# Optimization experiments

Measured on AMD Instinct MI355X. Metric: run time of the kernel, lower is better.

Reference implementation:

```python
import jax, jax.numpy as jnp
import numpy as np

N = 100000   # nodes
E = 1600000  # edges
DIN, DH, DOUT = 64, 128, 128


def setup_inputs() -> dict:
    key = jax.random.key(0)
    ks = jax.random.split(key, 12)
    x = jax.random.normal(ks[0], (N, DIN), dtype=jnp.float32)
    edge_index = jax.random.randint(ks[1], (2, E), 0, N, dtype=jnp.int32)
    s = 1.0 / np.sqrt(DIN)
    W1 = jax.random.uniform(ks[2], (DIN, DH), jnp.float32, -s, s)
    b1 = jnp.zeros((DH,), jnp.float32)
    g1 = jnp.ones((DH,), jnp.float32)
    bt1 = jnp.zeros((DH,), jnp.float32)
    s2 = 1.0 / np.sqrt(DH)
    W2 = jax.random.uniform(ks[3], (DH, DOUT), jnp.float32, -s2, s2)
    b2 = jnp.zeros((DOUT,), jnp.float32)
    g2 = jnp.ones((DOUT,), jnp.float32)
    bt2 = jnp.zeros((DOUT,), jnp.float32)
    return {"x": x, "edge_index": edge_index, "W1": W1, "b1": b1, "g1": g1,
            "bt1": bt1, "W2": W2, "b2": b2, "g2": g2, "bt2": bt2}


def _layer_norm(h, g, b, eps=1e-5):
    mu = h.mean(-1, keepdims=True)
    var = h.var(-1, keepdims=True)
    return (h - mu) * jax.lax.rsqrt(var + eps) * g + b


def reference(x, edge_index, W1, b1, g1, bt1, W2, b2, g2, bt2):
    # GCN normalization with self-loops (shared graph structure for both layers)
    src, dst = edge_index[0], edge_index[1]
    loops = jnp.arange(N, dtype=src.dtype)
    src = jnp.concatenate([src, loops])
    dst = jnp.concatenate([dst, loops])
    deg = jax.ops.segment_sum(jnp.ones_like(src, jnp.float32), dst, num_segments=N)
    dinv = jnp.where(deg > 0, jax.lax.rsqrt(deg), 0.0)
    norm = dinv[src] * dinv[dst]  # [E+N]

    def gcn(h, W, b):
        hw = h @ W                         # linear first (PyG GCNConv)
        msg = hw[src] * norm[:, None]      # gather + edge scale
        return jax.ops.segment_sum(msg, dst, num_segments=N) + b

    h = jax.nn.relu(_layer_norm(gcn(x, W1, b1), g1, bt1))
    # dropout is identity at inference
    h = jax.nn.relu(_layer_norm(gcn(h, W2, b2), g2, bt2))
    return h
```

## Files before the change

kernel.cpp:

```cpp
#include <hip/hip_runtime.h>

#define NN 100000
#define NE 1600000
#define NBKT 196
#define CAP 12288
#define EPB 8192
#define ABLK ((NE + EPB - 1) / EPB)
typedef unsigned short u16;
typedef unsigned int u32;

typedef __attribute__((ext_vector_type(8))) short short8v;
typedef __attribute__((ext_vector_type(4))) float f32x4;

__device__ __forceinline__ u32 f2bf(float f) {
    u32 u = __float_as_uint(f);
    return (u + 0x7fffu + ((u >> 16) & 1u)) >> 16;
}
__device__ __forceinline__ u32 pack2(float a, float b) {
    return f2bf(a) | (f2bf(b) << 16);
}
__device__ __forceinline__ void accum8(float* a, uint4 u, float w) {
    a[0] += __uint_as_float(u.x << 16) * w;
    a[1] += __uint_as_float(u.x & 0xffff0000u) * w;
    a[2] += __uint_as_float(u.y << 16) * w;
    a[3] += __uint_as_float(u.y & 0xffff0000u) * w;
    a[4] += __uint_as_float(u.z << 16) * w;
    a[5] += __uint_as_float(u.z & 0xffff0000u) * w;
    a[6] += __uint_as_float(u.w << 16) * w;
    a[7] += __uint_as_float(u.w & 0xffff0000u) * w;
}

__global__ __launch_bounds__(256) void kA_bin(const int* __restrict__ src,
                                              const int* __restrict__ dst,
                                              int* __restrict__ gcnt,
                                              u32* __restrict__ binned) {
    __shared__ int bc[NBKT];
    __shared__ int cbase[NBKT];
    const int tid = threadIdx.x;
    for (int i = tid; i < NBKT; i += 256) bc[i] = 0;
    __syncthreads();
    const int e0 = blockIdx.x * EPB;
#pragma unroll
    for (int i = 0; i < EPB / 256; ++i) {
        const int e = e0 + i * 256 + tid;
        if (e < NE) atomicAdd(&bc[dst[e] >> 9], 1);
    }
    __syncthreads();
    for (int i = tid; i < NBKT; i += 256)
        cbase[i] = bc[i] ? atomicAdd(&gcnt[i], bc[i]) : 0;
    __syncthreads();
    for (int i = tid; i < NBKT; i += 256) bc[i] = 0;
    __syncthreads();
#pragma unroll
    for (int i = 0; i < EPB / 256; ++i) {
        const int e = e0 + i * 256 + tid;
        if (e < NE) {
            const int d = dst[e];
            const int bkt = d >> 9;
            const int p = atomicAdd(&bc[bkt], 1);
            binned[bkt * CAP + cbase[bkt] + p] = ((u32)src[e] << 9) | (u32)(d & 511);
        }
    }
}

__global__ __launch_bounds__(256) void kB_fill(const u32* __restrict__ binned,
                                               const int* __restrict__ gcnt,
                                               int2* __restrict__ off2,
                                               float* __restrict__ dinv,
                                               int* __restrict__ csr) {
    __shared__ int lcnt[512];
    __shared__ int lpos[512];
    __shared__ int ws[4];
    const int b = blockIdx.x;
    const int tid = threadIdx.x;
    const int cnt = gcnt[b];
    const int base0 = b * CAP;
    const int node0 = b << 9;
    lcnt[tid] = 0;
    lcnt[tid + 256] = 0;
    __syncthreads();
    for (int e = tid; e < cnt; e += 256)
        atomicAdd(&lcnt[binned[base0 + e] & 511], 1);
    __syncthreads();
    const int c0 = lcnt[tid * 2], c1 = lcnt[tid * 2 + 1];
    const int s = c0 + c1;
    const int lane = tid & 63, w = tid >> 6;
    int incl = s;
#pragma unroll
    for (int o = 1; o < 64; o <<= 1) {
        const int u = __shfl_up(incl, o);
        if (lane >= o) incl += u;
    }
    if (lane == 63) ws[w] = incl;
    __syncthreads();
    int base = incl - s;
    for (int i = 0; i < w; ++i) base += ws[i];
    lpos[tid * 2] = base;
    lpos[tid * 2 + 1] = base + c0;
    const int n0 = node0 + tid * 2;
    if (n0 < NN) {
        off2[n0] = make_int2(base0 + base, base0 + base + c0);
        dinv[n0] = rsqrtf(1.0f + (float)c0);
    }
    if (n0 + 1 < NN) {
        off2[n0 + 1] = make_int2(base0 + base + c0, base0 + base + c0 + c1);
        dinv[n0 + 1] = rsqrtf(1.0f + (float)c1);
    }
    __syncthreads();
    for (int e = tid; e < cnt; e += 256) {
        const u32 u = binned[base0 + e];
        const int p = atomicAdd(&lpos[u & 511], 1);
        csr[base0 + p] = (int)(u >> 9);
    }
}

__global__ __launch_bounds__(256) void k_cvt(const float* __restrict__ x,
                                             const float* __restrict__ dinv,
                                             u16* __restrict__ xb) {
    const int i = blockIdx.x * 256 + threadIdx.x;
    if (i < NN * 8) {
        const int row = i >> 3;
        const float dr = dinv[row];
        const float4 v0 = *(const float4*)&x[(size_t)i * 8];
        const float4 v1 = *(const float4*)&x[(size_t)i * 8 + 4];
        uint4 o;
        o.x = pack2(v0.x * dr, v0.y * dr); o.y = pack2(v0.z * dr, v0.w * dr);
        o.z = pack2(v1.x * dr, v1.y * dr); o.w = pack2(v1.z * dr, v1.w * dr);
        *(uint4*)&xb[(size_t)i * 8] = o;
    }
}

__global__ __launch_bounds__(256) void k_wt(const float* __restrict__ W,
                                            u16* __restrict__ WT, int K) {
    const int i = blockIdx.x * 256 + threadIdx.x;
    if (i < K * 128) {
        const int k = i >> 7, c = i & 127;
        WT[c * K + k] = (u16)f2bf(W[i]);
    }
}

__global__ __launch_bounds__(256) void k_agg64(const u16* __restrict__ A,
                                               const int2* __restrict__ off2,
                                               const int* __restrict__ csr,
                                               const float* __restrict__ dinv,
                                               u16* __restrict__ out) {
    const int node = blockIdx.x * 4 + (threadIdx.x >> 6);
    const int lane = threadIdx.x & 63;
    const int sub = lane >> 3, l = lane & 7;
    const u32 coff = (u32)l << 4;
    const char* Ab = (const char*)A;
    const float di = dinv[node];
    float a[8] = {};
    {
        const uint4 u = *(const uint4*)(Ab + (u32)node * 128u + coff);
        accum8(a, u, (sub == 0) ? 1.0f : 0.0f);
    }
    const int2 oe = off2[node];
    int base = oe.x;
    const int e1 = oe.y;
    u32 iA = 0, iB = 0;
    float vA = 0.f, vB = 0.f;
    if (base < e1) {
        const int eA = base + sub, eB = base + sub + 8;
        iA = (u32)csr[min(eA, e1 - 1)];
        iB = (u32)csr[min(eB, e1 - 1)];
        vA = (eA < e1) ? 1.f : 0.f;
        vB = (eB < e1) ? 1.f : 0.f;
    }
    while (base < e1) {
        const uint4 uA = *(const uint4*)(Ab + iA * 128u + coff);
        const uint4 uB = *(const uint4*)(Ab + iB * 128u + coff);
        const float wA = vA, wB = vB;
        base += 16;
        if (base < e1) {
            const int eA = base + sub, eB = base + sub + 8;
            iA = (u32)csr[min(eA, e1 - 1)];
            iB = (u32)csr[min(eB, e1 - 1)];
            vA = (eA < e1) ? 1.f : 0.f;
            vB = (eB < e1) ? 1.f : 0.f;
        }
        accum8(a, uA, wA);
        accum8(a, uB, wB);
    }
#pragma unroll
    for (int i = 0; i < 8; ++i) {
        a[i] += __shfl_xor(a[i], 8);
        a[i] += __shfl_xor(a[i], 16);
        a[i] += __shfl_xor(a[i], 32);
    }
    if (sub == 0) {
        uint4 o;
        o.x = pack2(a[0] * di, a[1] * di); o.y = pack2(a[2] * di, a[3] * di);
        o.z = pack2(a[4] * di, a[5] * di); o.w = pack2(a[6] * di, a[7] * di);
        *(uint4*)((char*)out + (u32)node * 128u + coff) = o;
    }
}

__global__ __launch_bounds__(256) void k_agg128(const u16* __restrict__ A,
                                                const int2* __restrict__ off2,
                                                const int* __restrict__ csr,
                                                const float* __restrict__ dinv,
                                                u16* __restrict__ out) {
    const int node = blockIdx.x * 4 + (threadIdx.x >> 6);
    const int lane = threadIdx.x & 63;
    const int sub = lane >> 4, l = lane & 15;
    const u32 coff = (u32)l << 4;
    const char* Ab = (const char*)A;
    const float di = dinv[node];
    float a[8] = {};
    {
        const uint4 u = *(const uint4*)(Ab + ((u32)node << 8) + coff);
        accum8(a, u, (sub == 0) ? 1.0f : 0.0f);
    }
    const int2 oe = off2[node];
    int base = oe.x;
    const int e1 = oe.y;
    u32 iA = 0, iB = 0;
    float vA = 0.f, vB = 0.f;
    if (base < e1) {
        const int eA = base + sub, eB = base + sub + 4;
        iA = (u32)csr[min(eA, e1 - 1)];
        iB = (u32)csr[min(eB, e1 - 1)];
        vA = (eA < e1) ? 1.f : 0.f;
        vB = (eB < e1) ? 1.f : 0.f;
    }
    while (base < e1) {
        const uint4 uA = *(const uint4*)(Ab + (iA << 8) + coff);
        const uint4 uB = *(const uint4*)(Ab + (iB << 8) + coff);
        const float wA = vA, wB = vB;
        base += 8;
        if (base < e1) {
            const int eA = base + sub, eB = base + sub + 4;
            iA = (u32)csr[min(eA, e1 - 1)];
            iB = (u32)csr[min(eB, e1 - 1)];
            vA = (eA < e1) ? 1.f : 0.f;
            vB = (eB < e1) ? 1.f : 0.f;
        }
        accum8(a, uA, wA);
        accum8(a, uB, wB);
    }
#pragma unroll
    for (int i = 0; i < 8; ++i) {
        a[i] += __shfl_xor(a[i], 16);
        a[i] += __shfl_xor(a[i], 32);
    }
    if (sub == 0) {
        uint4 o;
        o.x = pack2(a[0] * di, a[1] * di); o.y = pack2(a[2] * di, a[3] * di);
        o.z = pack2(a[4] * di, a[5] * di); o.w = pack2(a[6] * di, a[7] * di);
        *(uint4*)((char*)out + ((u32)node << 8) + coff) = o;
    }
}

template<int K, bool FP32OUT, bool PRESCALE>
__global__ __launch_bounds__(256) void k_gemm_ln(const u16* __restrict__ Ain,
                                                 const u16* __restrict__ WT,
                                                 const float* __restrict__ bias,
                                                 const float* __restrict__ g,
                                                 const float* __restrict__ bt,
                                                 const float* __restrict__ dinv,
                                                 void* __restrict__ outp) {
    const int tid = threadIdx.x;
    const int wv = tid >> 6, lane = tid & 63;
    const int lr = lane & 15, kg = lane >> 4;
    const int row0 = blockIdx.x * 128 + wv * 32;

    short8v af[2][K / 32];
#pragma unroll
    for (int rt = 0; rt < 2; ++rt) {
        const int r = min(row0 + rt * 16 + lr, NN - 1);
#pragma unroll
        for (int kk = 0; kk < K / 32; ++kk)
            af[rt][kk] = *(const short8v*)&Ain[(size_t)r * K + kk * 32 + kg * 8];
    }
    f32x4 acc[2][8];
#pragma unroll
    for (int rt = 0; rt < 2; ++rt)
#pragma unroll
        for (int nt = 0; nt < 8; ++nt)
            acc[rt][nt] = (f32x4){0.f, 0.f, 0.f, 0.f};

#pragma unroll
    for (int nt = 0; nt < 8; ++nt) {
        const int col = nt * 16 + lr;
        short8v bf[K / 32];
#pragma unroll
        for (int kk = 0; kk < K / 32; ++kk)
            bf[kk] = *(const short8v*)&WT[col * K + kk * 32 + kg * 8];
#pragma unroll
        for (int rt = 0; rt < 2; ++rt)
#pragma unroll
            for (int kk = 0; kk < K / 32; ++kk)
                acc[rt][nt] = __builtin_amdgcn_mfma_f32_16x16x32_bf16(
                    af[rt][kk], bf[kk], acc[rt][nt], 0, 0, 0);
    }

    float bv[8], gv[8], tv[8];
#pragma unroll
    for (int nt = 0; nt < 8; ++nt) {
        const int col = nt * 16 + lr;
        bv[nt] = bias[col]; gv[nt] = g[col]; tv[nt] = bt[col];
    }

#pragma unroll
    for (int rt = 0; rt < 2; ++rt) {
        float s1[4] = {0.f, 0.f, 0.f, 0.f};
        float s2[4] = {0.f, 0.f, 0.f, 0.f};
#pragma unroll
        for (int nt = 0; nt < 8; ++nt)
#pragma unroll
            for (int j = 0; j < 4; ++j) {
                const float v = acc[rt][nt][j] + bv[nt];
                acc[rt][nt][j] = v;
                s1[j] += v;
                s2[j] += v * v;
            }
#pragma unroll
        for (int j = 0; j < 4; ++j)
#pragma unroll
            for (int o = 1; o < 16; o <<= 1) {
                s1[j] += __shfl_xor(s1[j], o);
                s2[j] += __shfl_xor(s2[j], o);
            }
#pragma unroll
        for (int j = 0; j < 4; ++j) {
            const int r = row0 + rt * 16 + kg * 4 + j;
            const float mu = s1[j] * (1.0f / 128.0f);
            const float var = s2[j] * (1.0f / 128.0f) - mu * mu;
            const float rs = rsqrtf(var + 1e-5f);
            if (r < NN) {
                const float dr = PRESCALE ? dinv[r] : 1.0f;
#pragma unroll
                for (int nt = 0; nt < 8; ++nt) {
                    const float y = fmaxf((acc[rt][nt][j] - mu) * rs * gv[nt] + tv[nt], 0.f) * dr;
                    const int col = nt * 16 + lr;
                    if constexpr (FP32OUT)
                        ((float*)outp)[(size_t)r * 128 + col] = y;
                    else
                        ((u16*)outp)[(size_t)r * 128 + col] = (u16)f2bf(y);
                }
            }
        }
    }
}

extern "C" void kernel_launch(void* const* d_in, const int* in_sizes, int n_in,
                              void* d_out, int out_size, void* d_ws, size_t ws_size,
                              hipStream_t stream) {
    const float* x   = (const float*)d_in[0];
    const int*   ei  = (const int*)d_in[1];
    const float* W1  = (const float*)d_in[2];
    const float* b1  = (const float*)d_in[3];
    const float* g1  = (const float*)d_in[4];
    const float* bt1 = (const float*)d_in[5];
    const float* W2  = (const float*)d_in[6];
    const float* b2  = (const float*)d_in[7];
    const float* g2  = (const float*)d_in[8];
    const float* bt2 = (const float*)d_in[9];

    const int* src = ei;
    const int* dst = ei + NE;

    const int NP = (NN + 255) & ~255;
    int*   gcnt  = (int*)d_ws;
    int2*  off2  = (int2*)(gcnt + 256);
    float* dinv  = (float*)(off2 + NP);
    int*   csr   = (int*)(dinv + NP);
    u32*   binR  = (u32*)(csr + NBKT * CAP);
    u16*   xb    = (u16*)(binR + (size_t)NN * 32);
    u16*   aggh  = xb + (size_t)NN * 64;
    u16*   WT1   = aggh + (size_t)NN * 128;
    u16*   WT2   = WT1 + 128 * 64;
    u32*   binned = binR;
    u16*   aggx  = (u16*)binR;
    u16*   h1    = (u16*)d_out;

    hipMemsetAsync(gcnt, 0, NBKT * sizeof(int), stream);
    kA_bin<<<ABLK, 256, 0, stream>>>(src, dst, gcnt, binned);
    kB_fill<<<NBKT, 256, 0, stream>>>(binned, gcnt, off2, dinv, csr);

    k_cvt<<<(NN * 8 + 255) / 256, 256, 0, stream>>>(x, dinv, xb);
    k_wt<<<(64 * 128 + 255) / 256, 256, 0, stream>>>(W1, WT1, 64);
    k_wt<<<(128 * 128 + 255) / 256, 256, 0, stream>>>(W2, WT2, 128);

    k_agg64<<<NN / 4, 256, 0, stream>>>(xb, off2, csr, dinv, aggx);
    k_gemm_ln<64, false, true><<<(NN + 127) / 128, 256, 0, stream>>>(
        aggx, WT1, b1, g1, bt1, dinv, h1);

    k_agg128<<<NN / 4, 256, 0, stream>>>(h1, off2, csr, dinv, aggh);
    k_gemm_ln<128, true, false><<<(NN + 127) / 128, 256, 0, stream>>>(
        aggh, WT2, b2, g2, bt2, dinv, d_out);
}
```

Baseline: 216.4 us.

## Pad CSR rows to multiples of four and gather four neighbors per lane

```diff
diff --git a/kernel.cpp b/kernel.cpp
--- a/kernel.cpp
+++ b/kernel.cpp
@@ -28,6 +28,16 @@
     a[5] += __uint_as_float(u.z & 0xffff0000u) * w;
     a[6] += __uint_as_float(u.w << 16) * w;
     a[7] += __uint_as_float(u.w & 0xffff0000u) * w;
+}
+__device__ __forceinline__ void accum8a(float* a, uint4 u) {
+    a[0] += __uint_as_float(u.x << 16);
+    a[1] += __uint_as_float(u.x & 0xffff0000u);
+    a[2] += __uint_as_float(u.y << 16);
+    a[3] += __uint_as_float(u.y & 0xffff0000u);
+    a[4] += __uint_as_float(u.z << 16);
+    a[5] += __uint_as_float(u.z & 0xffff0000u);
+    a[6] += __uint_as_float(u.w << 16);
+    a[7] += __uint_as_float(u.w & 0xffff0000u);
 }
 
 __global__ __launch_bounds__(256) void kA_bin(const int* __restrict__ src,
@@ -83,7 +93,9 @@
         atomicAdd(&lcnt[binned[base0 + e] & 511], 1);
     __syncthreads();
     const int c0 = lcnt[tid * 2], c1 = lcnt[tid * 2 + 1];
-    const int s = c0 + c1;
+    const int a0 = (c0 + 3) & ~3;
+    const int a1 = (c1 + 3) & ~3;
+    const int s = a0 + a1;
     const int lane = tid & 63, w = tid >> 6;
     int incl = s;
 #pragma unroll
@@ -96,16 +108,20 @@
     int base = incl - s;
     for (int i = 0; i < w; ++i) base += ws[i];
     lpos[tid * 2] = base;
-    lpos[tid * 2 + 1] = base + c0;
+    lpos[tid * 2 + 1] = base + a0;
     const int n0 = node0 + tid * 2;
     if (n0 < NN) {
         off2[n0] = make_int2(base0 + base, base0 + base + c0);
         dinv[n0] = rsqrtf(1.0f + (float)c0);
     }
     if (n0 + 1 < NN) {
-        off2[n0 + 1] = make_int2(base0 + base + c0, base0 + base + c0 + c1);
+        off2[n0 + 1] = make_int2(base0 + base + a0, base0 + base + a0 + c1);
         dinv[n0 + 1] = rsqrtf(1.0f + (float)c1);
     }
+    for (int k = c0; k < a0; ++k) csr[base0 + base + k] = 0;
+    for (int k = c1; k < a1; ++k) csr[base0 + base + a0 + k] = 0;
+    const int total = ws[0] + ws[1] + ws[2] + ws[3];
+    if (tid < 32) csr[base0 + total + tid] = 0;
     __syncthreads();
     for (int e = tid; e < cnt; e += 256) {
         const u32 u = binned[base0 + e];
@@ -147,40 +163,32 @@
     const int node = blockIdx.x * 4 + (threadIdx.x >> 6);
     const int lane = threadIdx.x & 63;
     const int sub = lane >> 3, l = lane & 7;
-    const u32 coff = (u32)l << 4;
-    const char* Ab = (const char*)A;
+    const char* Ab = (const char*)A + ((u32)l << 4);
     const float di = dinv[node];
     float a[8] = {};
     {
-        const uint4 u = *(const uint4*)(Ab + (u32)node * 128u + coff);
+        const uint4 u = *(const uint4*)(Ab + ((u32)node << 7));
         accum8(a, u, (sub == 0) ? 1.0f : 0.0f);
     }
     const int2 oe = off2[node];
-    int base = oe.x;
+    int e = oe.x;
     const int e1 = oe.y;
-    u32 iA = 0, iB = 0;
-    float vA = 0.f, vB = 0.f;
-    if (base < e1) {
-        const int eA = base + sub, eB = base + sub + 8;
-        iA = (u32)csr[min(eA, e1 - 1)];
-        iB = (u32)csr[min(eB, e1 - 1)];
-        vA = (eA < e1) ? 1.f : 0.f;
-        vB = (eB < e1) ? 1.f : 0.f;
-    }
-    while (base < e1) {
-        const uint4 uA = *(const uint4*)(Ab + iA * 128u + coff);
-        const uint4 uB = *(const uint4*)(Ab + iB * 128u + coff);
-        const float wA = vA, wB = vB;
-        base += 16;
-        if (base < e1) {
-            const int eA = base + sub, eB = base + sub + 8;
-            iA = (u32)csr[min(eA, e1 - 1)];
-            iB = (u32)csr[min(eB, e1 - 1)];
-            vA = (eA < e1) ? 1.f : 0.f;
-            vB = (eB < e1) ? 1.f : 0.f;
+    while (e < e1) {
+        const int4 ce = *(const int4*)&csr[e + 4 * sub];
+        const uint4 u0 = *(const uint4*)(Ab + ((u32)ce.x << 7));
+        const uint4 u1 = *(const uint4*)(Ab + ((u32)ce.y << 7));
+        const uint4 u2 = *(const uint4*)(Ab + ((u32)ce.z << 7));
+        const uint4 u3 = *(const uint4*)(Ab + ((u32)ce.w << 7));
+        if (e + 32 <= e1) {
+            accum8a(a, u0); accum8a(a, u1); accum8a(a, u2); accum8a(a, u3);
+        } else {
+            const int eb = e + 4 * sub;
+            accum8(a, u0, (eb + 0 < e1) ? 1.f : 0.f);
+            accum8(a, u1, (eb + 1 < e1) ? 1.f : 0.f);
+            accum8(a, u2, (eb + 2 < e1) ? 1.f : 0.f);
+            accum8(a, u3, (eb + 3 < e1) ? 1.f : 0.f);
         }
-        accum8(a, uA, wA);
-        accum8(a, uB, wB);
+        e += 32;
     }
 #pragma unroll
     for (int i = 0; i < 8; ++i) {
@@ -192,7 +200,7 @@
         uint4 o;
         o.x = pack2(a[0] * di, a[1] * di); o.y = pack2(a[2] * di, a[3] * di);
         o.z = pack2(a[4] * di, a[5] * di); o.w = pack2(a[6] * di, a[7] * di);
-        *(uint4*)((char*)out + (u32)node * 128u + coff) = o;
+        *(uint4*)((char*)out + ((u32)node << 7) + ((u32)l << 4)) = o;
     }
 }
 
@@ -204,40 +212,32 @@
     const int node = blockIdx.x * 4 + (threadIdx.x >> 6);
     const int lane = threadIdx.x & 63;
     const int sub = lane >> 4, l = lane & 15;
-    const u32 coff = (u32)l << 4;
-    const char* Ab = (const char*)A;
+    const char* Ab = (const char*)A + ((u32)l << 4);
     const float di = dinv[node];
     float a[8] = {};
     {
-        const uint4 u = *(const uint4*)(Ab + ((u32)node << 8) + coff);
+        const uint4 u = *(const uint4*)(Ab + ((u32)node << 8));
         accum8(a, u, (sub == 0) ? 1.0f : 0.0f);
     }
     const int2 oe = off2[node];
-    int base = oe.x;
+    int e = oe.x;
     const int e1 = oe.y;
-    u32 iA = 0, iB = 0;
-    float vA = 0.f, vB = 0.f;
-    if (base < e1) {
-        const int eA = base + sub, eB = base + sub + 4;
-        iA = (u32)csr[min(eA, e1 - 1)];
-        iB = (u32)csr[min(eB, e1 - 1)];
-        vA = (eA < e1) ? 1.f : 0.f;
-        vB = (eB < e1) ? 1.f : 0.f;
-    }
-    while (base < e1) {
-        const uint4 uA = *(const uint4*)(Ab + (iA << 8) + coff);
-        const uint4 uB = *(const uint4*)(Ab + (iB << 8) + coff);
-        const float wA = vA, wB = vB;
-        base += 8;
-        if (base < e1) {
-            const int eA = base + sub, eB = base + sub + 4;
-            iA = (u32)csr[min(eA, e1 - 1)];
-            iB = (u32)csr[min(eB, e1 - 1)];
-            vA = (eA < e1) ? 1.f : 0.f;
-            vB = (eB < e1) ? 1.f : 0.f;
+    while (e < e1) {
+        const int4 ce = *(const int4*)&csr[e + 4 * sub];
+        const uint4 u0 = *(const uint4*)(Ab + ((u32)ce.x << 8));
+        const uint4 u1 = *(const uint4*)(Ab + ((u32)ce.y << 8));
+        const uint4 u2 = *(const uint4*)(Ab + ((u32)ce.z << 8));
+        const uint4 u3 = *(const uint4*)(Ab + ((u32)ce.w << 8));
+        if (e + 16 <= e1) {
+            accum8a(a, u0); accum8a(a, u1); accum8a(a, u2); accum8a(a, u3);
+        } else {
+            const int eb = e + 4 * sub;
+            accum8(a, u0, (eb + 0 < e1) ? 1.f : 0.f);
+            accum8(a, u1, (eb + 1 < e1) ? 1.f : 0.f);
+            accum8(a, u2, (eb + 2 < e1) ? 1.f : 0.f);
+            accum8(a, u3, (eb + 3 < e1) ? 1.f : 0.f);
         }
-        accum8(a, uA, wA);
-        accum8(a, uB, wB);
+        e += 16;
     }
 #pragma unroll
     for (int i = 0; i < 8; ++i) {
@@ -248,7 +248,7 @@
         uint4 o;
         o.x = pack2(a[0] * di, a[1] * di); o.y = pack2(a[2] * di, a[3] * di);
         o.z = pack2(a[4] * di, a[5] * di); o.w = pack2(a[6] * di, a[7] * di);
-        *(uint4*)((char*)out + ((u32)node << 8) + coff) = o;
+        *(uint4*)((char*)out + ((u32)node << 8) + ((u32)l << 4)) = o;
     }
 }
 
```

New measurement: 224.0 us. 1.04x slower.
